# Performance work log

Measured on AMD Instinct MI355X. Metric: run time of the kernel, lower is better.

## Reference

```python
import jax, jax.numpy as jnp
import numpy as np

E, IN, H1, H2, H3, A, B = 20, 512, 1024, 512, 256, 32, 4096


def setup_inputs() -> dict:
    key = jax.random.key(0)
    ks = jax.random.split(key, 10)

    def w(k, shape, fan_in):
        return jax.random.normal(k, shape, dtype=jnp.float32) / np.sqrt(fan_in)

    return {
        "obs": jax.random.normal(ks[0], (B, IN), dtype=jnp.float32),
        # stacked expert MLP params [E, ...]
        "eW1": w(ks[1], (E, IN, H1), IN), "eb1": jnp.zeros((E, H1), jnp.float32),
        "eW2": w(ks[2], (E, H1, H2), H1), "eb2": jnp.zeros((E, H2), jnp.float32),
        "eW3": w(ks[3], (E, H2, H3), H2), "eb3": jnp.zeros((E, H3), jnp.float32),
        "eW4": w(ks[4], (E, H3, A), H3), "eb4": jnp.zeros((E, A), jnp.float32),
        # gate MLP params
        "gW1": w(ks[5], (IN, H1), IN), "gb1": jnp.zeros((H1,), jnp.float32),
        "gW2": w(ks[6], (H1, H2), H1), "gb2": jnp.zeros((H2,), jnp.float32),
        "gW3": w(ks[7], (H2, H3), H2), "gb3": jnp.zeros((H3,), jnp.float32),
        "gW4": w(ks[8], (H3, E), H3), "gb4": jnp.zeros((E,), jnp.float32),
    }


def _experts(obs, eW1, eb1, eW2, eb2, eW3, eb3, eW4, eb4):
    # batched over experts: [B, E, h]
    h = jax.nn.elu(jnp.einsum('bi,eih->beh', obs, eW1) + eb1[None])
    h = jax.nn.elu(jnp.einsum('beh,ehk->bek', h, eW2) + eb2[None])
    h = jax.nn.elu(jnp.einsum('bek,ekm->bem', h, eW3) + eb3[None])
    return jnp.einsum('bem,ema->bea', h, eW4) + eb4[None]  # [B, E, A]


def _gate(obs, gW1, gb1, gW2, gb2, gW3, gb3, gW4, gb4):
    h = jax.nn.elu(obs @ gW1 + gb1)
    h = jax.nn.elu(h @ gW2 + gb2)
    h = jax.nn.elu(h @ gW3 + gb3)
    return jax.nn.softmax(h @ gW4 + gb4, axis=-1)  # [B, E]


def reference(obs, eW1, eb1, eW2, eb2, eW3, eb3, eW4, eb4,
              gW1, gb1, gW2, gb2, gW3, gb3, gW4, gb4):
    weights = _gate(obs, gW1, gb1, gW2, gb2, gW3, gb3, gW4, gb4)       # [B, E]
    actions = _experts(obs, eW1, eb1, eW2, eb2, eW3, eb3, eW4, eb4)    # [B, E, A]
    # bmm(weights[:,None,:], actions).squeeze(1)
    return jnp.einsum('be,bea->ba', weights, actions)                   # [B, A]
```

## Files before the change

### kernel.cpp

```cpp
#include <hip/hip_runtime.h>

#define B_SZ 4096
#define E_EXP 20
#define NE 21

typedef unsigned short u16;
typedef __bf16 bf16x8 __attribute__((ext_vector_type(8)));
typedef u16 u16x8 __attribute__((ext_vector_type(8)));
typedef u16 u16x4 __attribute__((ext_vector_type(4)));
typedef float floatx4 __attribute__((ext_vector_type(4)));

static __device__ __forceinline__ u16 f2bf(float f) {
  unsigned u = __builtin_bit_cast(unsigned, f);
  u += 0x7fffu + ((u >> 16) & 1u);
  return (u16)(u >> 16);
}

static __device__ __forceinline__ float elu1(float v) {
  return v > 0.f ? v : (__expf(v) - 1.f);
}

static __device__ __forceinline__ bf16x8 ld_bf8(const u16* p) {
  u16x8 v = *reinterpret_cast<const u16x8*>(p);
  return __builtin_bit_cast(bf16x8, v);
}

static __device__ __forceinline__ void gld_lds16(const u16* g, u16* l) {
  __builtin_amdgcn_global_load_lds(
      (const __attribute__((address_space(1))) unsigned int*)g,
      (__attribute__((address_space(3))) unsigned int*)l, 16, 0, 0);
}


__global__ void prep_small_kernel(
    const float* __restrict__ obs, u16* __restrict__ obs_bf,
    const float* __restrict__ eb1, const float* __restrict__ gb1,
    const float* __restrict__ eb2, const float* __restrict__ gb2,
    const float* __restrict__ eb3, const float* __restrict__ gb3,
    float* __restrict__ b1, float* __restrict__ b2, float* __restrict__ b3) {
  int bid = blockIdx.x;
  if (bid < 2048) {
    int i = (bid * 256 + threadIdx.x) * 4;
    float4 v = *reinterpret_cast<const float4*>(obs + i);
    u16x4 o;
    o.x = f2bf(v.x); o.y = f2bf(v.y); o.z = f2bf(v.z); o.w = f2bf(v.w);
    *reinterpret_cast<u16x4*>(obs_bf + i) = o;
  } else {
    int i = (bid - 2048) * 256 + threadIdx.x;
    const int S1 = NE * 1024, S2 = NE * 512, S3 = NE * 256;
    if (i < S1) {
      b1[i] = (i < E_EXP * 1024) ? eb1[i] : gb1[i - E_EXP * 1024];
    } else if (i < S1 + S2) {
      int j = i - S1;
      b2[j] = (j < E_EXP * 512) ? eb2[j] : gb2[j - E_EXP * 512];
    } else if (i < S1 + S2 + S3) {
      int j = i - S1 - S2;
      b3[j] = (j < E_EXP * 256) ? eb3[j] : gb3[j - E_EXP * 256];
    }
  }
}

#define TRANS_BLOCKS 6132

__global__ __launch_bounds__(256) void transpose_all_kernel(
    const float* __restrict__ eW1, const float* __restrict__ gW1,
    const float* __restrict__ eW2, const float* __restrict__ gW2,
    const float* __restrict__ eW3, const float* __restrict__ gW3,
    const float* __restrict__ eW4, const float* __restrict__ gW4,
    u16* __restrict__ W1t, u16* __restrict__ W2t, u16* __restrict__ W3t,
    u16* __restrict__ W4t, u16* __restrict__ gW4t) {
  int f = blockIdx.x;
  const float *srcE, *srcG;
  u16* dstBase;
  int rem, K, N, Nout, kxt, tpm, nm;
  if (f < 2688) {
    rem = f;        srcE = eW1; srcG = gW1; dstBase = W1t;
    K = 512;  N = 1024; Nout = 1024; kxt = 8;  tpm = 128; nm = 20;
  } else if (f < 5376) {
    rem = f - 2688; srcE = eW2; srcG = gW2; dstBase = W2t;
    K = 1024; N = 512;  Nout = 512;  kxt = 16; tpm = 128; nm = 20;
  } else if (f < 6048) {
    rem = f - 5376; srcE = eW3; srcG = gW3; dstBase = W3t;
    K = 512;  N = 256;  Nout = 256;  kxt = 8;  tpm = 32;  nm = 20;
  } else if (f < 6128) {
    rem = f - 6048; srcE = eW4; srcG = nullptr; dstBase = W4t;
    K = 256;  N = 32;   Nout = 32;   kxt = 4;  tpm = 4;   nm = 99;
  } else {
    rem = f - 6128; srcE = gW4; srcG = nullptr; dstBase = gW4t;
    K = 256;  N = 20;   Nout = 32;   kxt = 4;  tpm = 4;   nm = 99;
  }
  int mat = rem / tpm;
  int t = rem % tpm;
  const float* src = (mat < nm) ? (srcE + (long)mat * K * N) : srcG;
  u16* dst = dstBase + (long)mat * Nout * K;
  int kbase = (t % kxt) * 64;
  int nbase = (t / kxt) * 64;

  __shared__ float tl[64][65];
  int tid = threadIdx.x;
  int kk = tid >> 4;
  int n4 = (tid & 15) * 4;
#pragma unroll
  for (int p = 0; p < 4; ++p) {
    int k = kbase + p * 16 + kk;
    int n = nbase + n4;
    float4 v = make_float4(0.f, 0.f, 0.f, 0.f);
    if (n + 3 < N) {
      v = *reinterpret_cast<const float4*>(&src[(long)k * N + n]);
    } else {
      float* vp = &v.x;
      for (int j = 0; j < 4; ++j)
        if (n + j < N) vp[j] = src[(long)k * N + n + j];
    }
    tl[p * 16 + kk][n4 + 0] = v.x;
    tl[p * 16 + kk][n4 + 1] = v.y;
    tl[p * 16 + kk][n4 + 2] = v.z;
    tl[p * 16 + kk][n4 + 3] = v.w;
  }
  __syncthreads();

  int kk8 = (tid & 7) * 8;
#pragma unroll
  for (int p = 0; p < 2; ++p) {
    int ln = p * 32 + (tid >> 3);
    int n = nbase + ln;
    if (n < Nout) {
      u16x8 o;
#pragma unroll
      for (int j = 0; j < 8; ++j) o[j] = f2bf(tl[kk8 + j][ln]);
      *reinterpret_cast<u16x8*>(&dst[(long)n * K + kbase + kk8]) = o;
    }
  }
}


#define BM 256
#define BN 128

__global__ __launch_bounds__(256, 2) void gemm_bias_elu_kernel(
    const u16* __restrict__ A_base, long a_estride,
    const u16* __restrict__ Wt_base, long w_estride,
    const float* __restrict__ bias_base, long b_estride,
    u16* __restrict__ C_base, long c_estride,
    int M, int N, int K) {
  int e = blockIdx.z;
  const u16* A = A_base + (long)e * a_estride;
  const u16* Wt = Wt_base + (long)e * w_estride;
  const float* bias = bias_base + (long)e * b_estride;
  u16* C = C_base + (long)e * c_estride;

  int m0 = blockIdx.y * BM;
  int n0 = blockIdx.x * BN;

  __shared__ u16 As[2 * BM * 32];
  __shared__ u16 Bs[2 * BN * 32];

  int tid = threadIdx.x;
  int lane = tid & 63;
  int w = tid >> 6;
  int wm = (w >> 1) * 128;
  int wn = (w & 1) * 64;
  int col = lane & 15;
  int quad = lane >> 4;

  floatx4 acc[8][4] = {};

  int srow = tid >> 2;
  int scol = (tid & 3) * 8;
  const u16* gA = &A[(long)(m0 + srow) * K + scol];
  const u16* gB = &Wt[(long)(n0 + srow) * K + scol];

  for (int k0 = 0; k0 < K; k0 += 64) {
    __syncthreads();
    gld_lds16(gA + k0,                 &As[(size_t)tid * 8]);
    gld_lds16(gA + (long)64 * K + k0,  &As[2048 + (size_t)tid * 8]);
    gld_lds16(gA + (long)128 * K + k0, &As[4096 + (size_t)tid * 8]);
    gld_lds16(gA + (long)192 * K + k0, &As[6144 + (size_t)tid * 8]);
    gld_lds16(gA + k0 + 32,                 &As[8192 + (size_t)tid * 8]);
    gld_lds16(gA + (long)64 * K + k0 + 32,  &As[10240 + (size_t)tid * 8]);
    gld_lds16(gA + (long)128 * K + k0 + 32, &As[12288 + (size_t)tid * 8]);
    gld_lds16(gA + (long)192 * K + k0 + 32, &As[14336 + (size_t)tid * 8]);
    gld_lds16(gB + k0,                &Bs[(size_t)tid * 8]);
    gld_lds16(gB + (long)64 * K + k0, &Bs[2048 + (size_t)tid * 8]);
    gld_lds16(gB + k0 + 32,                &Bs[4096 + (size_t)tid * 8]);
    gld_lds16(gB + (long)64 * K + k0 + 32, &Bs[6144 + (size_t)tid * 8]);
    __syncthreads();

#pragma unroll
    for (int kk = 0; kk < 2; ++kk) {
      bf16x8 xf[8], wf[4];
#pragma unroll
      for (int t = 0; t < 8; ++t)
        xf[t] = __builtin_bit_cast(bf16x8,
            *reinterpret_cast<u16x8*>(
                &As[kk * 8192 + (wm + t * 16 + col) * 32 + quad * 8]));
#pragma unroll
      for (int t = 0; t < 4; ++t)
        wf[t] = __builtin_bit_cast(bf16x8,
            *reinterpret_cast<u16x8*>(
                &Bs[kk * 4096 + (wn + t * 16 + col) * 32 + quad * 8]));
#pragma unroll
      for (int i = 0; i < 8; ++i)
#pragma unroll
        for (int j = 0; j < 4; ++j)
          acc[i][j] = __builtin_amdgcn_mfma_f32_16x16x32_bf16(
              wf[j], xf[i], acc[i][j], 0, 0, 0);
    }
  }

#pragma unroll
  for (int j = 0; j < 4; ++j) {
    int nn = n0 + wn + j * 16 + quad * 4;
    float4 b4 = *reinterpret_cast<const float4*>(&bias[nn]);
#pragma unroll
    for (int i = 0; i < 8; ++i) {
      int m = m0 + wm + i * 16 + col;
      u16x4 o;
      o.x = f2bf(elu1(acc[i][j][0] + b4.x));
      o.y = f2bf(elu1(acc[i][j][1] + b4.y));
      o.z = f2bf(elu1(acc[i][j][2] + b4.z));
      o.w = f2bf(elu1(acc[i][j][3] + b4.w));
      *reinterpret_cast<u16x4*>(&C[(long)m * N + nn]) = o;
    }
  }
}

__global__ __launch_bounds__(256) void final_combine_kernel(
    const u16* __restrict__ h3, const u16* __restrict__ W4t,
    const u16* __restrict__ gW4t, const float* __restrict__ eb4,
    const float* __restrict__ gb4, float* __restrict__ out) {
  const int H3 = 256;
  int tid = threadIdx.x;
  int lane = tid & 63;
  int w = tid >> 6;
  int col = lane & 15;
  int quad = lane >> 4;
  int r0 = blockIdx.x * 16;

  floatx4 g0 = {}, g1 = {};
  const u16* h3g = h3 + (long)E_EXP * B_SZ * H3;
#pragma unroll
  for (int k0 = 0; k0 < 256; k0 += 32) {
    bf16x8 a = ld_bf8(&h3g[(long)(r0 + col) * H3 + k0 + quad * 8]);
    bf16x8 b0 = ld_bf8(&gW4t[(long)col * H3 + k0 + quad * 8]);
    bf16x8 b1 = ld_bf8(&gW4t[(long)(16 + col) * H3 + k0 + quad * 8]);
    g0 = __builtin_amdgcn_mfma_f32_16x16x32_bf16(a, b0, g0, 0, 0, 0);
    g1 = __builtin_amdgcn_mfma_f32_16x16x32_bf16(a, b1, g1, 0, 0, 0);
  }

  float w0[4], w1[4];
  float gbc0 = gb4[col];
  float gbc1 = (col < 4) ? gb4[16 + col] : 0.f;
#pragma unroll
  for (int r = 0; r < 4; ++r) {
    float v0 = g0[r] + gbc0;
    float v1 = (col < 4) ? (g1[r] + gbc1) : -1e30f;
    float m = fmaxf(v0, v1);
#pragma unroll
    for (int s = 1; s < 16; s <<= 1) m = fmaxf(m, __shfl_xor(m, s, 64));
    float e0 = __expf(v0 - m);
    float e1 = (col < 4) ? __expf(v1 - m) : 0.f;
    float ssum = e0 + e1;
#pragma unroll
    for (int s = 1; s < 16; s <<= 1) ssum += __shfl_xor(ssum, s, 64);
    w0[r] = e0 / ssum;
    w1[r] = e1 / ssum;
  }

  floatx4 o0 = {}, o1 = {};
  for (int e = w; e < E_EXP; e += 4) {
    floatx4 a0 = {}, a1 = {};
    const u16* he = h3 + (long)e * B_SZ * H3;
    const u16* we = W4t + (long)e * 32 * H3;
#pragma unroll
    for (int k0 = 0; k0 < 256; k0 += 32) {
      bf16x8 a = ld_bf8(&he[(long)(r0 + col) * H3 + k0 + quad * 8]);
      bf16x8 b0 = ld_bf8(&we[(long)col * H3 + k0 + quad * 8]);
      bf16x8 b1 = ld_bf8(&we[(long)(16 + col) * H3 + k0 + quad * 8]);
      a0 = __builtin_amdgcn_mfma_f32_16x16x32_bf16(a, b0, a0, 0, 0, 0);
      a1 = __builtin_amdgcn_mfma_f32_16x16x32_bf16(a, b1, a1, 0, 0, 0);
    }
    float be0 = eb4[e * 32 + col];
    float be1 = eb4[e * 32 + 16 + col];
    int src = (lane & 48) + (e & 15);
#pragma unroll
    for (int r = 0; r < 4; ++r) {
      float wr = __shfl((e < 16) ? w0[r] : w1[r], src, 64);
      o0[r] += wr * (a0[r] + be0);
      o1[r] += wr * (a1[r] + be1);
    }
  }

  __shared__ float red[3][64][8];
  if (w > 0) {
#pragma unroll
    for (int r = 0; r < 4; ++r) {
      red[w - 1][lane][r] = o0[r];
      red[w - 1][lane][4 + r] = o1[r];
    }
  }
  __syncthreads();
  if (w == 0) {
#pragma unroll
    for (int ww = 0; ww < 3; ++ww)
#pragma unroll
      for (int r = 0; r < 4; ++r) {
        o0[r] += red[ww][lane][r];
        o1[r] += red[ww][lane][4 + r];
      }
#pragma unroll
    for (int r = 0; r < 4; ++r) {
      int row = r0 + quad * 4 + r;
      out[(long)row * 32 + col] = o0[r];
      out[(long)row * 32 + 16 + col] = o1[r];
    }
  }
}


static inline size_t align256(size_t x) { return (x + 255) & ~(size_t)255; }

extern "C" void kernel_launch(void* const* d_in, const int* in_sizes, int n_in,
                              void* d_out, int out_size, void* d_ws,
                              size_t ws_size, hipStream_t stream) {
  const float* obs = (const float*)d_in[0];
  const float* eW1 = (const float*)d_in[1];
  const float* eb1 = (const float*)d_in[2];
  const float* eW2 = (const float*)d_in[3];
  const float* eb2 = (const float*)d_in[4];
  const float* eW3 = (const float*)d_in[5];
  const float* eb3 = (const float*)d_in[6];
  const float* eW4 = (const float*)d_in[7];
  const float* eb4 = (const float*)d_in[8];
  const float* gW1 = (const float*)d_in[9];
  const float* gb1 = (const float*)d_in[10];
  const float* gW2 = (const float*)d_in[11];
  const float* gb2 = (const float*)d_in[12];
  const float* gW3 = (const float*)d_in[13];
  const float* gb3 = (const float*)d_in[14];
  const float* gW4 = (const float*)d_in[15];
  const float* gb4 = (const float*)d_in[16];
  float* out = (float*)d_out;
  char* ws = (char*)d_ws;

  size_t off = 0;
  size_t OFF_OBS = off;  off = align256(off + (size_t)B_SZ * 512 * 2);
  size_t OFF_W1T = off;  off = align256(off + (size_t)NE * 1024 * 512 * 2);
  size_t OFF_W2T = off;  off = align256(off + (size_t)NE * 512 * 1024 * 2);
  size_t OFF_W3T = off;  off = align256(off + (size_t)NE * 256 * 512 * 2);
  size_t OFF_W4T = off;  off = align256(off + (size_t)E_EXP * 32 * 256 * 2);
  size_t OFF_GW4T = off; off = align256(off + (size_t)32 * 256 * 2);
  size_t OFF_B1 = off;   off = align256(off + (size_t)NE * 1024 * 4);
  size_t OFF_B2 = off;   off = align256(off + (size_t)NE * 512 * 4);
  size_t OFF_B3 = off;   off = align256(off + (size_t)NE * 256 * 4);
  size_t OFF_H3 = off;   off = align256(off + (size_t)NE * B_SZ * 256 * 2);

  int chunk = B_SZ;
  size_t OFF_H1 = off;
  while (chunk > 512) {
    size_t need = (size_t)NE * chunk * 1024 * 2 + (size_t)NE * chunk * 512 * 2;
    if (OFF_H1 + need <= ws_size) break;
    chunk >>= 1;
  }
  size_t OFF_H2 = align256(OFF_H1 + (size_t)NE * chunk * 1024 * 2);

  u16* obs_bf = (u16*)(ws + OFF_OBS);
  u16* W1t = (u16*)(ws + OFF_W1T);
  u16* W2t = (u16*)(ws + OFF_W2T);
  u16* W3t = (u16*)(ws + OFF_W3T);
  u16* W4t = (u16*)(ws + OFF_W4T);
  u16* gW4t = (u16*)(ws + OFF_GW4T);
  float* b1 = (float*)(ws + OFF_B1);
  float* b2 = (float*)(ws + OFF_B2);
  float* b3 = (float*)(ws + OFF_B3);
  u16* h3 = (u16*)(ws + OFF_H3);
  u16* h1 = (u16*)(ws + OFF_H1);
  u16* h2 = (u16*)(ws + OFF_H2);

  prep_small_kernel<<<2048 + (NE * 1792 + 255) / 256, 256, 0, stream>>>(
      obs, obs_bf, eb1, gb1, eb2, gb2, eb3, gb3, b1, b2, b3);
  transpose_all_kernel<<<TRANS_BLOCKS, 256, 0, stream>>>(
      eW1, gW1, eW2, gW2, eW3, gW3, eW4, gW4, W1t, W2t, W3t, W4t, gW4t);

  for (int bc = 0; bc < B_SZ; bc += chunk) {
    gemm_bias_elu_kernel<<<dim3(1024 / BN, chunk / BM, NE), 256, 0, stream>>>(
        obs_bf + (size_t)bc * 512, 0L,
        W1t, (long)1024 * 512,
        b1, 1024L,
        h1, (long)chunk * 1024, chunk, 1024, 512);
    gemm_bias_elu_kernel<<<dim3(512 / BN, chunk / BM, NE), 256, 0, stream>>>(
        h1, (long)chunk * 1024,
        W2t, (long)512 * 1024,
        b2, 512L,
        h2, (long)chunk * 512, chunk, 512, 1024);
    gemm_bias_elu_kernel<<<dim3(256 / BN, chunk / BM, NE), 256, 0, stream>>>(
        h2, (long)chunk * 512,
        W3t, (long)256 * 512,
        b3, 256L,
        h3 + (size_t)bc * 256, (long)B_SZ * 256, chunk, 256, 512);
  }

  final_combine_kernel<<<B_SZ / 16, 256, 0, stream>>>(h3, W4t, gW4t, eb4, gb4,
                                                      out);
}
```

Measured before the change: 557.9 us.

## Prefetch GEMM tiles through registers and shrink block M tile to 128

The batched bias+ELU GEMM now loads the next K-slice of A and W into registers while the MFMAs run on the current slice in LDS. This replaces the direct global-to-LDS loads, which left the load latency exposed on every iteration. The M tile is halved to 128 and launch bounds raised to 4 blocks per CU. This gives more blocks and lower register pressure per block, at the cost of less data reuse per block. It also adds an extra register-to-LDS store step.

New measurement: 664.7 us. 19.1% more time.

```diff
diff --git a/kernel.cpp b/kernel.cpp
--- a/kernel.cpp
+++ b/kernel.cpp
@@ -23,12 +23,6 @@
 static __device__ __forceinline__ bf16x8 ld_bf8(const u16* p) {
   u16x8 v = *reinterpret_cast<const u16x8*>(p);
   return __builtin_bit_cast(bf16x8, v);
-}
-
-static __device__ __forceinline__ void gld_lds16(const u16* g, u16* l) {
-  __builtin_amdgcn_global_load_lds(
-      (const __attribute__((address_space(1))) unsigned int*)g,
-      (__attribute__((address_space(3))) unsigned int*)l, 16, 0, 0);
 }
 
 
@@ -134,10 +128,10 @@
 }
 
 
-#define BM 256
+#define BM 128
 #define BN 128
 
-__global__ __launch_bounds__(256, 2) void gemm_bias_elu_kernel(
+__global__ __launch_bounds__(256, 4) void gemm_bias_elu_kernel(
     const u16* __restrict__ A_base, long a_estride,
     const u16* __restrict__ Wt_base, long w_estride,
     const float* __restrict__ bias_base, long b_estride,
@@ -158,49 +152,68 @@
   int tid = threadIdx.x;
   int lane = tid & 63;
   int w = tid >> 6;
-  int wm = (w >> 1) * 128;
+  int wm = (w >> 1) * 64;
   int wn = (w & 1) * 64;
   int col = lane & 15;
   int quad = lane >> 4;
 
-  floatx4 acc[8][4] = {};
+  floatx4 acc[4][4] = {};
 
   int srow = tid >> 2;
   int scol = (tid & 3) * 8;
   const u16* gA = &A[(long)(m0 + srow) * K + scol];
   const u16* gB = &Wt[(long)(n0 + srow) * K + scol];
+  long rowK = (long)64 * K;
+
+  u16x8 rA[4], rB[4];
+  rA[0] = *reinterpret_cast<const u16x8*>(gA);
+  rA[1] = *reinterpret_cast<const u16x8*>(gA + rowK);
+  rA[2] = *reinterpret_cast<const u16x8*>(gA + 32);
+  rA[3] = *reinterpret_cast<const u16x8*>(gA + rowK + 32);
+  rB[0] = *reinterpret_cast<const u16x8*>(gB);
+  rB[1] = *reinterpret_cast<const u16x8*>(gB + rowK);
+  rB[2] = *reinterpret_cast<const u16x8*>(gB + 32);
+  rB[3] = *reinterpret_cast<const u16x8*>(gB + rowK + 32);
 
   for (int k0 = 0; k0 < K; k0 += 64) {
     __syncthreads();
-    gld_lds16(gA + k0,                 &As[(size_t)tid * 8]);
-    gld_lds16(gA + (long)64 * K + k0,  &As[2048 + (size_t)tid * 8]);
-    gld_lds16(gA + (long)128 * K + k0, &As[4096 + (size_t)tid * 8]);
-    gld_lds16(gA + (long)192 * K + k0, &As[6144 + (size_t)tid * 8]);
-    gld_lds16(gA + k0 + 32,                 &As[8192 + (size_t)tid * 8]);
-    gld_lds16(gA + (long)64 * K + k0 + 32,  &As[10240 + (size_t)tid * 8]);
-    gld_lds16(gA + (long)128 * K + k0 + 32, &As[12288 + (size_t)tid * 8]);
-    gld_lds16(gA + (long)192 * K + k0 + 32, &As[14336 + (size_t)tid * 8]);
-    gld_lds16(gB + k0,                &Bs[(size_t)tid * 8]);
-    gld_lds16(gB + (long)64 * K + k0, &Bs[2048 + (size_t)tid * 8]);
-    gld_lds16(gB + k0 + 32,                &Bs[4096 + (size_t)tid * 8]);
-    gld_lds16(gB + (long)64 * K + k0 + 32, &Bs[6144 + (size_t)tid * 8]);
+    *reinterpret_cast<u16x8*>(&As[(size_t)tid * 8]) = rA[0];
+    *reinterpret_cast<u16x8*>(&As[(size_t)(256 + tid) * 8]) = rA[1];
+    *reinterpret_cast<u16x8*>(&As[(size_t)(512 + tid) * 8]) = rA[2];
+    *reinterpret_cast<u16x8*>(&As[(size_t)(768 + tid) * 8]) = rA[3];
+    *reinterpret_cast<u16x8*>(&Bs[(size_t)tid * 8]) = rB[0];
+    *reinterpret_cast<u16x8*>(&Bs[(size_t)(256 + tid) * 8]) = rB[1];
+    *reinterpret_cast<u16x8*>(&Bs[(size_t)(512 + tid) * 8]) = rB[2];
+    *reinterpret_cast<u16x8*>(&Bs[(size_t)(768 + tid) * 8]) = rB[3];
     __syncthreads();
 
+    if (k0 + 64 < K) {
+      const u16* pA = gA + k0 + 64;
+      const u16* pB = gB + k0 + 64;
+      rA[0] = *reinterpret_cast<const u16x8*>(pA);
+      rA[1] = *reinterpret_cast<const u16x8*>(pA + rowK);
+      rA[2] = *reinterpret_cast<const u16x8*>(pA + 32);
+      rA[3] = *reinterpret_cast<const u16x8*>(pA + rowK + 32);
+      rB[0] = *reinterpret_cast<const u16x8*>(pB);
+      rB[1] = *reinterpret_cast<const u16x8*>(pB + rowK);
+      rB[2] = *reinterpret_cast<const u16x8*>(pB + 32);
+      rB[3] = *reinterpret_cast<const u16x8*>(pB + rowK + 32);
+    }
+
 #pragma unroll
     for (int kk = 0; kk < 2; ++kk) {
-      bf16x8 xf[8], wf[4];
-#pragma unroll
-      for (int t = 0; t < 8; ++t)
+      bf16x8 xf[4], wf[4];
+#pragma unroll
+      for (int t = 0; t < 4; ++t) {
         xf[t] = __builtin_bit_cast(bf16x8,
             *reinterpret_cast<u16x8*>(
-                &As[kk * 8192 + (wm + t * 16 + col) * 32 + quad * 8]));
-#pragma unroll
-      for (int t = 0; t < 4; ++t)
+                &As[kk * BM * 32 + (wm + t * 16 + col) * 32 + quad * 8]));
         wf[t] = __builtin_bit_cast(bf16x8,
             *reinterpret_cast<u16x8*>(
-                &Bs[kk * 4096 + (wn + t * 16 + col) * 32 + quad * 8]));
-#pragma unroll
-      for (int i = 0; i < 8; ++i)
+                &Bs[kk * BN * 32 + (wn + t * 16 + col) * 32 + quad * 8]));
+      }
+#pragma unroll
+      for (int i = 0; i < 4; ++i)
 #pragma unroll
         for (int j = 0; j < 4; ++j)
           acc[i][j] = __builtin_amdgcn_mfma_f32_16x16x32_bf16(
@@ -213,7 +226,7 @@
     int nn = n0 + wn + j * 16 + quad * 4;
     float4 b4 = *reinterpret_cast<const float4*>(&bias[nn]);
 #pragma unroll
-    for (int i = 0; i < 8; ++i) {
+    for (int i = 0; i < 4; ++i) {
       int m = m0 + wm + i * 16 + col;
       u16x4 o;
       o.x = f2bf(elu1(acc[i][j][0] + b4.x));
```
